# Optimization experiments

Measured on AMD Instinct MI355X. Metric: run time of the kernel, lower is better.

## Reference

```python
import jax, jax.numpy as jnp
import numpy as np

N = 8192
E = 131072
IN = 512
H = 8
C = 128
HC = H * C
EPS = 1e-5
NEG_SLOPE = 0.2


def _gatv2(x, src, dst, Wl, bl, Wr, br, att, bias):
    """GATv2Conv (PyG semantics, concat=True, self-loops already in src/dst)."""
    n = x.shape[0]
    xl = (x @ Wl + bl).reshape(n, H, C)  # source transform (lin_l)
    xr = (x @ Wr + br).reshape(n, H, C)  # dest transform (lin_r)
    m = xl[src] + xr[dst]                # [E,H,C] per-edge message
    e = jnp.einsum('ehc,hc->eh', jax.nn.leaky_relu(m, NEG_SLOPE), att)  # [E,H]
    # segment softmax over destination nodes
    emax = jax.ops.segment_max(e, dst, num_segments=n)
    w = jnp.exp(e - emax[dst])
    denom = jax.ops.segment_sum(w, dst, num_segments=n)
    alpha = w / denom[dst]               # [E,H]
    out = jax.ops.segment_sum(alpha[:, :, None] * xl[src], dst, num_segments=n)
    return out.reshape(n, HC) + bias


def _bn(x, gamma, beta):
    mu = jnp.mean(x, axis=0)
    var = jnp.mean((x - mu) ** 2, axis=0)
    return (x - mu) * jax.lax.rsqrt(var + EPS) * gamma + beta


def setup_inputs() -> dict:
    key = jax.random.key(0)
    ks = jax.random.split(key, 16)
    s = 0.05
    return {
        'x': jax.random.normal(ks[0], (N, IN), jnp.float32),
        'edge_index': jax.random.randint(ks[1], (2, E), 0, N, jnp.int32),
        'W1l': jax.random.normal(ks[2], (IN, HC), jnp.float32) * s,
        'b1l': jnp.zeros((HC,), jnp.float32),
        'W1r': jax.random.normal(ks[3], (IN, HC), jnp.float32) * s,
        'b1r': jnp.zeros((HC,), jnp.float32),
        'att1': jax.random.normal(ks[4], (H, C), jnp.float32) * s,
        'bias1': jnp.zeros((HC,), jnp.float32),
        'g1': jnp.ones((HC,), jnp.float32),
        'beta1': jnp.zeros((HC,), jnp.float32),
        'W2l': jax.random.normal(ks[5], (HC, HC), jnp.float32) * s,
        'b2l': jnp.zeros((HC,), jnp.float32),
        'W2r': jax.random.normal(ks[6], (HC, HC), jnp.float32) * s,
        'b2r': jnp.zeros((HC,), jnp.float32),
        'att2': jax.random.normal(ks[7], (H, C), jnp.float32) * s,
        'bias2': jnp.zeros((HC,), jnp.float32),
        'g2': jnp.ones((HC,), jnp.float32),
        'beta2': jnp.zeros((HC,), jnp.float32),
    }


def reference(x, edge_index, W1l, b1l, W1r, b1r, att1, bias1, g1, beta1,
              W2l, b2l, W2r, b2r, att2, bias2, g2, beta2):
    n = x.shape[0]
    loops = jnp.arange(n, dtype=edge_index.dtype)
    src = jnp.concatenate([edge_index[0], loops])
    dst = jnp.concatenate([edge_index[1], loops])
    h = _gatv2(x, src, dst, W1l, b1l, W1r, b1r, att1, bias1)
    h = jax.nn.elu(_bn(h, g1, beta1))
    h = _gatv2(h, src, dst, W2l, b2l, W2r, b2r, att2, bias2)
    h = jax.nn.elu(_bn(h, g2, beta2))
    return h
```

## Files before the change

kernel.cpp:

```cpp
#include <hip/hip_runtime.h>
#include <stdint.h>

#define NN     8192
#define NEDGE  131072
#define NETOT  (NEDGE + NN)
#define K_IN   512
#define HC_    1024
#define NOUT   2048
#define BNEPS  1e-5f
#define SLOPE  0.2f

typedef __bf16 bf16x8 __attribute__((ext_vector_type(8)));
typedef float  f32x4  __attribute__((ext_vector_type(4)));

__device__ __forceinline__ float bf2f(unsigned short u) {
  union { uint32_t u; float f; } c; c.u = ((uint32_t)u) << 16; return c.f;
}
__device__ __forceinline__ unsigned short f2bf(float f) {
  union { float f; uint32_t u; } c; c.f = f;
  uint32_t r = c.u + 0x7fffu + ((c.u >> 16) & 1u);
  return (unsigned short)(r >> 16);
}
__device__ __forceinline__ void unpack2(uint32_t u, float& lo, float& hi) {
  union { uint32_t u; float f; } a, b;
  a.u = u << 16; b.u = u & 0xffff0000u;
  lo = a.f; hi = b.f;
}

__device__ __forceinline__ void gload16(const void* g, void* l) {
  __builtin_amdgcn_global_load_lds(
      (const __attribute__((address_space(1))) uint32_t*)g,
      (__attribute__((address_space(3))) uint32_t*)l, 16, 0, 0);
}

#define SBAR() do { asm volatile("" ::: "memory"); __builtin_amdgcn_s_barrier(); asm volatile("" ::: "memory"); } while (0)

__global__ __launch_bounds__(256) void k_cvt_bf16(const float* __restrict__ in,
                                                  unsigned short* __restrict__ out, int n4) {
  int i = blockIdx.x * 256 + threadIdx.x;
  if (i >= n4) return;
  float4 v = *(const float4*)&in[(size_t)i * 4];
  ushort4 o;
  o.x = f2bf(v.x); o.y = f2bf(v.y); o.z = f2bf(v.z); o.w = f2bf(v.w);
  *(ushort4*)&out[(size_t)i * 4] = o;
}

__global__ __launch_bounds__(256) void k_transpose2_bf16(const float* __restrict__ Wa,
                                                         const float* __restrict__ Wb,
                                                         unsigned short* __restrict__ Wt,
                                                         int K, int N) {
  __shared__ float tile[32][33];
  const float* W = blockIdx.z ? Wb : Wa;
  unsigned short* dst = Wt + (size_t)blockIdx.z * N * K;
  int n0 = blockIdx.x * 32, k0 = blockIdx.y * 32;
  int tx = threadIdx.x & 31, ty = threadIdx.x >> 5;
  for (int i = ty; i < 32; i += 8)
    tile[i][tx] = W[(size_t)(k0 + i) * N + n0 + tx];
  __syncthreads();
  for (int i = ty; i < 32; i += 8)
    dst[(size_t)(n0 + i) * K + k0 + tx] = f2bf(tile[tx][i]);
}

__global__ __launch_bounds__(256) void k_hist(const int* __restrict__ ei, int* __restrict__ cnt) {
  int i = blockIdx.x * 256 + threadIdx.x;
  if (i >= NETOT) return;
  int d = (i < NEDGE) ? ei[NEDGE + i] : (i - NEDGE);
  atomicAdd(&cnt[d], 1);
}

__global__ __launch_bounds__(256) void k_scan(const int* __restrict__ cnt,
                                              int* __restrict__ rowptr,
                                              int* __restrict__ cursor) {
  __shared__ int part[256];
  int t = threadIdx.x;
  int base = t * 32;
  int s = 0;
  for (int i = 0; i < 32; ++i) s += cnt[base + i];
  part[t] = s;
  __syncthreads();
  for (int off = 1; off < 256; off <<= 1) {
    int u = (t >= off) ? part[t - off] : 0;
    __syncthreads();
    part[t] += u;
    __syncthreads();
  }
  int run = part[t] - s;
  for (int i = 0; i < 32; ++i) {
    rowptr[base + i] = run;
    cursor[base + i] = run;
    run += cnt[base + i];
  }
  if (t == 255) rowptr[NN] = run;
}

__global__ __launch_bounds__(256) void k_scatter(const int* __restrict__ ei,
                                                 int* __restrict__ cursor,
                                                 int* __restrict__ srcs) {
  int i = blockIdx.x * 256 + threadIdx.x;
  if (i >= NETOT) return;
  int s, d;
  if (i < NEDGE) { s = ei[i]; d = ei[NEDGE + i]; }
  else           { s = d = i - NEDGE; }
  int pos = atomicAdd(&cursor[d], 1);
  srcs[pos] = s;
}

__global__ __launch_bounds__(512, 2) void k_gemm256(const unsigned short* __restrict__ A,
                                                    const unsigned short* __restrict__ Bt,
                                                    const float* __restrict__ biasL,
                                                    const float* __restrict__ biasR,
                                                    unsigned short* __restrict__ C,
                                                    int K) {
  __shared__ unsigned short lA[2][256 * 64];
  __shared__ unsigned short lB[2][256 * 64];

  const int bid = blockIdx.x;
  const int xcd = bid & 7, idx = bid >> 3;
  const int m0 = (xcd * 4 + (idx & 3)) * 256;
  const int n0 = (idx >> 2) * 256;

  const int tid = threadIdx.x;
  const int l   = tid & 63;
  const int wv  = tid >> 6;
  const int wm  = wv >> 2, wn = wv & 3;
  const int l15 = l & 15, l4 = l >> 4;

  const int srow = tid >> 3;
  const int ssgk = (tid & 7) ^ (srow & 7);

  const f32x4 vzero = {0.f, 0.f, 0.f, 0.f};
  f32x4 acc[8][4];
#pragma unroll
  for (int i = 0; i < 8; ++i)
#pragma unroll
    for (int j = 0; j < 4; ++j) acc[i][j] = vzero;

  bf16x8 a2[8];
  bf16x8 bb[2][4];

  auto stageA = [&](int kt, int h) {
    const int buf = kt & 1;
    const size_t go = (size_t)(m0 + h * 128 + srow) * K + (size_t)kt * 64 + ssgk * 8;
    unsigned short* lp = &lA[buf][h * 8192 + tid * 8];
    gload16(&A[go], lp);
    gload16(&A[go + (size_t)64 * K], lp + 4096);
  };
  auto stageB = [&](int kt, int h) {
    const int buf = kt & 1;
    const size_t go = (size_t)(n0 + h * 128 + srow) * K + (size_t)kt * 64 + ssgk * 8;
    unsigned short* lp = &lB[buf][h * 8192 + tid * 8];
    gload16(&Bt[go], lp);
    gload16(&Bt[go + (size_t)64 * K], lp + 4096);
  };
  auto readA = [&](int buf, int qm) {
#pragma unroll
    for (int fm = 0; fm < 4; ++fm)
#pragma unroll
      for (int kk = 0; kk < 2; ++kk) {
        int r = wm * 128 + (qm * 4 + fm) * 16 + l15;
        int g = (kk * 4 + l4) ^ (r & 7);
        a2[fm * 2 + kk] = *(const bf16x8*)&lA[buf][r * 64 + g * 8];
      }
  };
  auto readB = [&](int buf, int qn) {
#pragma unroll
    for (int fn = 0; fn < 2; ++fn)
#pragma unroll
      for (int kk = 0; kk < 2; ++kk) {
        int r = wn * 64 + (qn * 2 + fn) * 16 + l15;
        int g = (kk * 4 + l4) ^ (r & 7);
        bb[qn][fn * 2 + kk] = *(const bf16x8*)&lB[buf][r * 64 + g * 8];
      }
  };
  auto quad = [&](int qm, int qn) {
    __builtin_amdgcn_s_setprio(1);
#pragma unroll
    for (int fm = 0; fm < 4; ++fm)
#pragma unroll
      for (int fn = 0; fn < 2; ++fn)
#pragma unroll
        for (int kk = 0; kk < 2; ++kk)
          acc[qm * 4 + fm][qn * 2 + fn] = __builtin_amdgcn_mfma_f32_16x16x32_bf16(
              a2[fm * 2 + kk], bb[qn][fn * 2 + kk], acc[qm * 4 + fm][qn * 2 + fn], 0, 0, 0);
    __builtin_amdgcn_s_setprio(0);
  };

  const int NT = K >> 6;

  stageA(0, 0); stageA(0, 1); stageB(0, 0); stageB(0, 1);
  if (NT > 1) stageA(1, 0);
  asm volatile("s_waitcnt vmcnt(2)" ::: "memory");
  SBAR();

  for (int t = 0; t < NT; ++t) {
    const int buf = t & 1;
    readA(buf, 0); readB(buf, 0);
    if (t + 1 < NT) stageA(t + 1, 1);
    SBAR();
    quad(0, 0);
    SBAR();
    readB(buf, 1);
    if (t + 1 < NT) stageB(t + 1, 0);
    SBAR();
    quad(0, 1);
    SBAR();
    readA(buf, 1);
    if (t + 1 < NT) stageB(t + 1, 1);
    SBAR();
    quad(1, 0);
    SBAR();
    if (t + 2 < NT) stageA(t + 2, 0);
    asm volatile("s_waitcnt vmcnt(2)" ::: "memory");
    SBAR();
    quad(1, 1);
    SBAR();
  }

  const float* bias = (n0 < HC_) ? biasL : (biasR - HC_);
#pragma unroll
  for (int fm = 0; fm < 8; ++fm) {
#pragma unroll
    for (int fn = 0; fn < 4; ++fn) {
      int col = n0 + wn * 64 + fn * 16 + l15;
      float bv = bias[col];
#pragma unroll
      for (int j = 0; j < 4; ++j) {
        int row = m0 + wm * 128 + fm * 16 + l4 * 4 + j;
        C[(size_t)row * NOUT + col] = f2bf(acc[fm][fn][j] + bv);
      }
    }
  }
}

template <bool OUT_BF16>
__global__ __launch_bounds__(256) void k_edge_agg(const unsigned short* __restrict__ XLR,
                                                  const float* __restrict__ att,
                                                  const float* __restrict__ bias,
                                                  const int* __restrict__ rowptr,
                                                  const int* __restrict__ srcs,
                                                  void* __restrict__ outp) {
  const int tid = threadIdx.x;
  const int d   = blockIdx.x * 4 + (tid >> 6);
  const int l   = tid & 63;
  const int c0  = l * 16;

  float attv[16], xrv[16];
  {
    const float4* ap = (const float4*)&att[c0];
#pragma unroll
    for (int q = 0; q < 4; ++q) {
      float4 v = ap[q];
      attv[q * 4 + 0] = v.x; attv[q * 4 + 1] = v.y;
      attv[q * 4 + 2] = v.z; attv[q * 4 + 3] = v.w;
    }
    const uint4* rp = (const uint4*)&XLR[(size_t)d * NOUT + HC_ + c0];
    uint4 u0 = rp[0], u1 = rp[1];
    unpack2(u0.x, xrv[0], xrv[1]);   unpack2(u0.y, xrv[2], xrv[3]);
    unpack2(u0.z, xrv[4], xrv[5]);   unpack2(u0.w, xrv[6], xrv[7]);
    unpack2(u1.x, xrv[8], xrv[9]);   unpack2(u1.y, xrv[10], xrv[11]);
    unpack2(u1.z, xrv[12], xrv[13]); unpack2(u1.w, xrv[14], xrv[15]);
  }

  float acc[16];
#pragma unroll
  for (int j = 0; j < 16; ++j) acc[j] = 0.f;
  float den = 0.f;

  const int beg = rowptr[d], end = rowptr[d + 1];
  uint4 b0u0, b0u1, b1u0, b1u1;
  {
    const uint4* rp = (const uint4*)&XLR[(size_t)srcs[beg] * NOUT + c0];
    b0u0 = rp[0]; b0u1 = rp[1];
  }
  if (beg + 1 < end) {
    const uint4* rp = (const uint4*)&XLR[(size_t)srcs[beg + 1] * NOUT + c0];
    b1u0 = rp[0]; b1u1 = rp[1];
  }
  int s2 = (beg + 2 < end) ? srcs[beg + 2] : 0;

  for (int i = beg; i < end; ++i) {
    uint4 u0 = b0u0, u1 = b0u1;
    b0u0 = b1u0; b0u1 = b1u1;
    if (i + 2 < end) {
      const uint4* rp = (const uint4*)&XLR[(size_t)s2 * NOUT + c0];
      b1u0 = rp[0]; b1u1 = rp[1];
    }
    s2 = (i + 3 < end) ? srcs[i + 3] : 0;

    float x[16];
    unpack2(u0.x, x[0], x[1]);   unpack2(u0.y, x[2], x[3]);
    unpack2(u0.z, x[4], x[5]);   unpack2(u0.w, x[6], x[7]);
    unpack2(u1.x, x[8], x[9]);   unpack2(u1.y, x[10], x[11]);
    unpack2(u1.z, x[12], x[13]); unpack2(u1.w, x[14], x[15]);
    float p = 0.f;
#pragma unroll
    for (int j = 0; j < 16; ++j) {
      float m  = x[j] + xrv[j];
      float lr = fmaxf(m, SLOPE * m);
      p = fmaf(lr, attv[j], p);
    }
    p += __shfl_xor(p, 1);
    p += __shfl_xor(p, 2);
    p += __shfl_xor(p, 4);
    float wgt = __expf(p);
    den += wgt;
#pragma unroll
    for (int j = 0; j < 16; ++j) acc[j] = fmaf(wgt, x[j], acc[j]);
  }

  float inv = 1.0f / den;
  if (OUT_BF16) {
    unsigned short* op = (unsigned short*)outp + (size_t)d * HC_ + c0;
#pragma unroll
    for (int q = 0; q < 2; ++q) {
      ushort4 o0, o1;
      const float4 bv0 = ((const float4*)&bias[c0])[q * 2];
      const float4 bv1 = ((const float4*)&bias[c0])[q * 2 + 1];
      o0.x = f2bf(acc[q * 8 + 0] * inv + bv0.x); o0.y = f2bf(acc[q * 8 + 1] * inv + bv0.y);
      o0.z = f2bf(acc[q * 8 + 2] * inv + bv0.z); o0.w = f2bf(acc[q * 8 + 3] * inv + bv0.w);
      o1.x = f2bf(acc[q * 8 + 4] * inv + bv1.x); o1.y = f2bf(acc[q * 8 + 5] * inv + bv1.y);
      o1.z = f2bf(acc[q * 8 + 6] * inv + bv1.z); o1.w = f2bf(acc[q * 8 + 7] * inv + bv1.w);
      *(ushort4*)&op[q * 8]     = o0;
      *(ushort4*)&op[q * 8 + 4] = o1;
    }
  } else {
    float* op = (float*)outp + (size_t)d * HC_ + c0;
#pragma unroll
    for (int q = 0; q < 4; ++q) {
      float4 bv = ((const float4*)&bias[c0])[q];
      float4 o = {acc[q * 4 + 0] * inv + bv.x, acc[q * 4 + 1] * inv + bv.y,
                  acc[q * 4 + 2] * inv + bv.z, acc[q * 4 + 3] * inv + bv.w};
      *(float4*)&op[q * 4] = o;
    }
  }
}

template <bool IN_BF16>
__global__ __launch_bounds__(256) void k_colstats(const void* __restrict__ Xp,
                                                  float* __restrict__ stats) {
  int col = blockIdx.x * 256 + threadIdx.x;
  int r0 = blockIdx.y * 128;
  float s = 0.f, q = 0.f;
  for (int r = r0; r < r0 + 128; ++r) {
    float v = IN_BF16 ? bf2f(((const unsigned short*)Xp)[(size_t)r * HC_ + col])
                      : ((const float*)Xp)[(size_t)r * HC_ + col];
    s += v;
    q += v * v;
  }
  atomicAdd(&stats[col], s);
  atomicAdd(&stats[HC_ + col], q);
}

template <bool IN_BF16, bool OUT_BF16>
__global__ __launch_bounds__(256) void k_bn_elu(const void* __restrict__ Xp,
                                                const float* __restrict__ stats,
                                                const float* __restrict__ gamma,
                                                const float* __restrict__ beta,
                                                void* __restrict__ outp) {
  size_t idx = (size_t)blockIdx.x * 256 + threadIdx.x;
  size_t e0 = idx * 4;
  int col = (int)(e0 & (HC_ - 1));
  float xs[4];
  if (IN_BF16) {
    ushort4 u = *(const ushort4*)&((const unsigned short*)Xp)[e0];
    xs[0] = bf2f(u.x); xs[1] = bf2f(u.y); xs[2] = bf2f(u.z); xs[3] = bf2f(u.w);
  } else {
    float4 xv = *(const float4*)&((const float*)Xp)[e0];
    xs[0] = xv.x; xs[1] = xv.y; xs[2] = xv.z; xs[3] = xv.w;
  }
  float os[4];
  const float rn = 1.0f / (float)NN;
#pragma unroll
  for (int j = 0; j < 4; ++j) {
    int c = col + j;
    float mu = stats[c] * rn;
    float var = stats[HC_ + c] * rn - mu * mu;
    float v = (xs[j] - mu) * rsqrtf(var + BNEPS) * gamma[c] + beta[c];
    os[j] = v > 0.f ? v : (__expf(v) - 1.f);
  }
  if (OUT_BF16) {
    ushort4 o;
    o.x = f2bf(os[0]); o.y = f2bf(os[1]); o.z = f2bf(os[2]); o.w = f2bf(os[3]);
    *(ushort4*)&((unsigned short*)outp)[e0] = o;
  } else {
    float4 o = {os[0], os[1], os[2], os[3]};
    *(float4*)&((float*)outp)[e0] = o;
  }
}

extern "C" void kernel_launch(void* const* d_in, const int* in_sizes, int n_in,
                              void* d_out, int out_size, void* d_ws, size_t ws_size,
                              hipStream_t stream) {
  const float* x     = (const float*)d_in[0];
  const int*   ei    = (const int*)d_in[1];
  const float* W1l   = (const float*)d_in[2];
  const float* b1l   = (const float*)d_in[3];
  const float* W1r   = (const float*)d_in[4];
  const float* b1r   = (const float*)d_in[5];
  const float* att1  = (const float*)d_in[6];
  const float* bias1 = (const float*)d_in[7];
  const float* g1    = (const float*)d_in[8];
  const float* be1   = (const float*)d_in[9];
  const float* W2l   = (const float*)d_in[10];
  const float* b2l   = (const float*)d_in[11];
  const float* W2r   = (const float*)d_in[12];
  const float* b2r   = (const float*)d_in[13];
  const float* att2  = (const float*)d_in[14];
  const float* bias2 = (const float*)d_in[15];
  const float* g2    = (const float*)d_in[16];
  const float* be2   = (const float*)d_in[17];
  float* out = (float*)d_out;

  char* wsb = (char*)d_ws;
  size_t o = 0;
  auto alloc = [&](size_t b) {
    void* p = wsb + o;
    o = (o + b + 255) & ~(size_t)255;
    return p;
  };
  unsigned short* xbf  = (unsigned short*)alloc((size_t)NN * K_IN * 2);
  unsigned short* wT1  = (unsigned short*)alloc((size_t)NOUT * K_IN * 2);
  unsigned short* wT2  = (unsigned short*)alloc((size_t)NOUT * HC_ * 2);
  unsigned short* XLR  = (unsigned short*)alloc((size_t)NN * NOUT * 2);
  unsigned short* h0   = (unsigned short*)alloc((size_t)NN * HC_ * 2);
  int* cnt     = (int*)alloc((size_t)NN * 4);
  int* rowptr  = (int*)alloc((size_t)(NN + 1) * 4);
  int* cursor  = (int*)alloc((size_t)NN * 4);
  int* srcs    = (int*)alloc((size_t)NETOT * 4);
  float* stats = (float*)alloc((size_t)2 * HC_ * 4);

  hipMemsetAsync(cnt, 0, (size_t)NN * 4, stream);
  hipMemsetAsync(stats, 0, (size_t)2 * HC_ * 4, stream);

  k_cvt_bf16<<<(NN * K_IN / 4 + 255) / 256, 256, 0, stream>>>(x, xbf, NN * K_IN / 4);
  k_transpose2_bf16<<<dim3(HC_ / 32, K_IN / 32, 2), 256, 0, stream>>>(W1l, W1r, wT1, K_IN, HC_);
  k_transpose2_bf16<<<dim3(HC_ / 32, HC_ / 32, 2), 256, 0, stream>>>(W2l, W2r, wT2, HC_, HC_);

  k_hist<<<(NETOT + 255) / 256, 256, 0, stream>>>(ei, cnt);
  k_scan<<<1, 256, 0, stream>>>(cnt, rowptr, cursor);
  k_scatter<<<(NETOT + 255) / 256, 256, 0, stream>>>(ei, cursor, srcs);

  k_gemm256<<<256, 512, 0, stream>>>(xbf, wT1, b1l, b1r, XLR, K_IN);
  k_edge_agg<true><<<NN / 4, 256, 0, stream>>>(XLR, att1, bias1, rowptr, srcs, h0);
  k_colstats<true><<<dim3(HC_ / 256, NN / 128), 256, 0, stream>>>(h0, stats);
  k_bn_elu<true, true><<<NN * HC_ / 4 / 256, 256, 0, stream>>>(h0, stats, g1, be1, h0);

  k_gemm256<<<256, 512, 0, stream>>>(h0, wT2, b2l, b2r, XLR, HC_);
  k_edge_agg<false><<<NN / 4, 256, 0, stream>>>(XLR, att2, bias2, rowptr, srcs, out);
  hipMemsetAsync(stats, 0, (size_t)2 * HC_ * 4, stream);
  k_colstats<false><<<dim3(HC_ / 256, NN / 128), 256, 0, stream>>>(out, stats);
  k_bn_elu<false, false><<<NN * HC_ / 4 / 256, 256, 0, stream>>>(out, stats, g2, be2, out);
}
```

Before: 239.9 us.

## Deepen edge-gather prefetch, use packed float2 math, store layer-2 output as bf16

The edge aggregation loop now keeps three source rows in flight instead of two, using a three-way rotated unrolled loop. It also does the leaky-relu, attention dot product and accumulation on float2 vectors so the compiler can emit packed FP32 instructions. Separately, the layer-2 aggregation writes a bf16 intermediate that colstats and bn_elu then read, which cuts memory traffic but rounds the pre-BN values to bf16. The extra prefetch depth adds register pressure.

After: 248.6 us. 1.04x slower.

```diff
diff --git a/kernel.cpp b/kernel.cpp
--- a/kernel.cpp
+++ b/kernel.cpp
@@ -12,6 +12,7 @@
 
 typedef __bf16 bf16x8 __attribute__((ext_vector_type(8)));
 typedef float  f32x4  __attribute__((ext_vector_type(4)));
+typedef float  f32x2  __attribute__((ext_vector_type(2)));
 
 __device__ __forceinline__ float bf2f(unsigned short u) {
   union { uint32_t u; float f; } c; c.u = ((uint32_t)u) << 16; return c.f;
@@ -21,10 +22,10 @@
   uint32_t r = c.u + 0x7fffu + ((c.u >> 16) & 1u);
   return (unsigned short)(r >> 16);
 }
-__device__ __forceinline__ void unpack2(uint32_t u, float& lo, float& hi) {
+__device__ __forceinline__ f32x2 upk2(uint32_t u) {
   union { uint32_t u; float f; } a, b;
   a.u = u << 16; b.u = u & 0xffff0000u;
-  lo = a.f; hi = b.f;
+  f32x2 r; r.x = a.f; r.y = b.f; return r;
 }
 
 __device__ __forceinline__ void gload16(const void* g, void* l) {
@@ -244,93 +245,102 @@
   const int l   = tid & 63;
   const int c0  = l * 16;
 
-  float attv[16], xrv[16];
+  f32x2 attv[8], xrv[8];
   {
-    const float4* ap = (const float4*)&att[c0];
-#pragma unroll
-    for (int q = 0; q < 4; ++q) {
-      float4 v = ap[q];
-      attv[q * 4 + 0] = v.x; attv[q * 4 + 1] = v.y;
-      attv[q * 4 + 2] = v.z; attv[q * 4 + 3] = v.w;
-    }
+    const f32x2* ap = (const f32x2*)&att[c0];
+#pragma unroll
+    for (int q = 0; q < 8; ++q) attv[q] = ap[q];
     const uint4* rp = (const uint4*)&XLR[(size_t)d * NOUT + HC_ + c0];
     uint4 u0 = rp[0], u1 = rp[1];
-    unpack2(u0.x, xrv[0], xrv[1]);   unpack2(u0.y, xrv[2], xrv[3]);
-    unpack2(u0.z, xrv[4], xrv[5]);   unpack2(u0.w, xrv[6], xrv[7]);
-    unpack2(u1.x, xrv[8], xrv[9]);   unpack2(u1.y, xrv[10], xrv[11]);
-    unpack2(u1.z, xrv[12], xrv[13]); unpack2(u1.w, xrv[14], xrv[15]);
-  }
-
-  float acc[16];
-#pragma unroll
-  for (int j = 0; j < 16; ++j) acc[j] = 0.f;
+    xrv[0] = upk2(u0.x); xrv[1] = upk2(u0.y); xrv[2] = upk2(u0.z); xrv[3] = upk2(u0.w);
+    xrv[4] = upk2(u1.x); xrv[5] = upk2(u1.y); xrv[6] = upk2(u1.z); xrv[7] = upk2(u1.w);
+  }
+
+  f32x2 acc[8];
+#pragma unroll
+  for (int j = 0; j < 8; ++j) acc[j] = (f32x2){0.f, 0.f};
   float den = 0.f;
 
   const int beg = rowptr[d], end = rowptr[d + 1];
-  uint4 b0u0, b0u1, b1u0, b1u1;
+
+  uint4 A0, A1, B0, B1, C0, C1;
   {
     const uint4* rp = (const uint4*)&XLR[(size_t)srcs[beg] * NOUT + c0];
-    b0u0 = rp[0]; b0u1 = rp[1];
+    A0 = rp[0]; A1 = rp[1];
   }
   if (beg + 1 < end) {
     const uint4* rp = (const uint4*)&XLR[(size_t)srcs[beg + 1] * NOUT + c0];
-    b1u0 = rp[0]; b1u1 = rp[1];
-  }
-  int s2 = (beg + 2 < end) ? srcs[beg + 2] : 0;
-
-  for (int i = beg; i < end; ++i) {
-    uint4 u0 = b0u0, u1 = b0u1;
-    b0u0 = b1u0; b0u1 = b1u1;
-    if (i + 2 < end) {
-      const uint4* rp = (const uint4*)&XLR[(size_t)s2 * NOUT + c0];
-      b1u0 = rp[0]; b1u1 = rp[1];
-    }
-    s2 = (i + 3 < end) ? srcs[i + 3] : 0;
-
-    float x[16];
-    unpack2(u0.x, x[0], x[1]);   unpack2(u0.y, x[2], x[3]);
-    unpack2(u0.z, x[4], x[5]);   unpack2(u0.w, x[6], x[7]);
-    unpack2(u1.x, x[8], x[9]);   unpack2(u1.y, x[10], x[11]);
-    unpack2(u1.z, x[12], x[13]); unpack2(u1.w, x[14], x[15]);
-    float p = 0.f;
-#pragma unroll
-    for (int j = 0; j < 16; ++j) {
-      float m  = x[j] + xrv[j];
-      float lr = fmaxf(m, SLOPE * m);
-      p = fmaf(lr, attv[j], p);
-    }
-    p += __shfl_xor(p, 1);
-    p += __shfl_xor(p, 2);
-    p += __shfl_xor(p, 4);
-    float wgt = __expf(p);
-    den += wgt;
-#pragma unroll
-    for (int j = 0; j < 16; ++j) acc[j] = fmaf(wgt, x[j], acc[j]);
-  }
+    B0 = rp[0]; B1 = rp[1];
+  }
+  if (beg + 2 < end) {
+    const uint4* rp = (const uint4*)&XLR[(size_t)srcs[beg + 2] * NOUT + c0];
+    C0 = rp[0]; C1 = rp[1];
+  }
+  int sD = (beg + 3 < end) ? srcs[beg + 3] : 0;
+  int sE = (beg + 4 < end) ? srcs[beg + 4] : 0;
+
+  int i = beg;
+
+#define EDGE_STEP(X0, X1)                                                      \
+  {                                                                            \
+    f32x2 x[8];                                                                \
+    x[0] = upk2(X0.x); x[1] = upk2(X0.y); x[2] = upk2(X0.z); x[3] = upk2(X0.w);\
+    x[4] = upk2(X1.x); x[5] = upk2(X1.y); x[6] = upk2(X1.z); x[7] = upk2(X1.w);\
+    if (i + 3 < end) {                                                         \
+      const uint4* rp = (const uint4*)&XLR[(size_t)sD * NOUT + c0];            \
+      X0 = rp[0]; X1 = rp[1];                                                  \
+    }                                                                          \
+    sD = sE;                                                                   \
+    if (i + 5 < end) sE = srcs[i + 5];                                         \
+    f32x2 ps = (f32x2){0.f, 0.f};                                              \
+    _Pragma("unroll")                                                          \
+    for (int j = 0; j < 8; ++j) {                                              \
+      f32x2 y  = x[j] + xrv[j];                                                \
+      f32x2 lr = __builtin_elementwise_max(y, y * SLOPE);                      \
+      ps = lr * attv[j] + ps;                                                  \
+    }                                                                          \
+    float p = ps.x + ps.y;                                                     \
+    p += __shfl_xor(p, 1);                                                     \
+    p += __shfl_xor(p, 2);                                                     \
+    p += __shfl_xor(p, 4);                                                     \
+    float wgt = __expf(p);                                                     \
+    den += wgt;                                                                \
+    f32x2 w2 = (f32x2){wgt, wgt};                                              \
+    _Pragma("unroll")                                                          \
+    for (int j = 0; j < 8; ++j) acc[j] = w2 * x[j] + acc[j];                   \
+    ++i;                                                                       \
+  }
+
+  while (true) {
+    EDGE_STEP(A0, A1); if (i >= end) break;
+    EDGE_STEP(B0, B1); if (i >= end) break;
+    EDGE_STEP(C0, C1); if (i >= end) break;
+  }
+#undef EDGE_STEP
 
   float inv = 1.0f / den;
+  float o[16];
+#pragma unroll
+  for (int j = 0; j < 8; ++j) {
+    f32x2 bv = ((const f32x2*)&bias[c0])[j];
+    o[j * 2]     = acc[j].x * inv + bv.x;
+    o[j * 2 + 1] = acc[j].y * inv + bv.y;
+  }
   if (OUT_BF16) {
     unsigned short* op = (unsigned short*)outp + (size_t)d * HC_ + c0;
-#pragma unroll
-    for (int q = 0; q < 2; ++q) {
-      ushort4 o0, o1;
-      const float4 bv0 = ((const float4*)&bias[c0])[q * 2];
-      const float4 bv1 = ((const float4*)&bias[c0])[q * 2 + 1];
-      o0.x = f2bf(acc[q * 8 + 0] * inv + bv0.x); o0.y = f2bf(acc[q * 8 + 1] * inv + bv0.y);
-      o0.z = f2bf(acc[q * 8 + 2] * inv + bv0.z); o0.w = f2bf(acc[q * 8 + 3] * inv + bv0.w);
-      o1.x = f2bf(acc[q * 8 + 4] * inv + bv1.x); o1.y = f2bf(acc[q * 8 + 5] * inv + bv1.y);
-      o1.z = f2bf(acc[q * 8 + 6] * inv + bv1.z); o1.w = f2bf(acc[q * 8 + 7] * inv + bv1.w);
-      *(ushort4*)&op[q * 8]     = o0;
-      *(ushort4*)&op[q * 8 + 4] = o1;
+    ushort4 u[4];
+#pragma unroll
+    for (int q = 0; q < 4; ++q) {
+      u[q].x = f2bf(o[q * 4 + 0]); u[q].y = f2bf(o[q * 4 + 1]);
+      u[q].z = f2bf(o[q * 4 + 2]); u[q].w = f2bf(o[q * 4 + 3]);
+      *(ushort4*)&op[q * 4] = u[q];
     }
   } else {
     float* op = (float*)outp + (size_t)d * HC_ + c0;
 #pragma unroll
     for (int q = 0; q < 4; ++q) {
-      float4 bv = ((const float4*)&bias[c0])[q];
-      float4 o = {acc[q * 4 + 0] * inv + bv.x, acc[q * 4 + 1] * inv + bv.y,
-                  acc[q * 4 + 2] * inv + bv.z, acc[q * 4 + 3] * inv + bv.w};
-      *(float4*)&op[q * 4] = o;
+      float4 ov = {o[q * 4 + 0], o[q * 4 + 1], o[q * 4 + 2], o[q * 4 + 3]};
+      *(float4*)&op[q * 4] = ov;
     }
   }
 }
@@ -446,8 +456,8 @@
   k_bn_elu<true, true><<<NN * HC_ / 4 / 256, 256, 0, stream>>>(h0, stats, g1, be1, h0);
 
   k_gemm256<<<256, 512, 0, stream>>>(h0, wT2, b2l, b2r, XLR, HC_);
-  k_edge_agg<false><<<NN / 4, 256, 0, stream>>>(XLR, att2, bias2, rowptr, srcs, out);
+  k_edge_agg<true><<<NN / 4, 256, 0, stream>>>(XLR, att2, bias2, rowptr, srcs, h0);
   hipMemsetAsync(stats, 0, (size_t)2 * HC_ * 4, stream);
-  k_colstats<false><<<dim3(HC_ / 256, NN / 128), 256, 0, stream>>>(out, stats);
-  k_bn_elu<false, false><<<NN * HC_ / 4 / 256, 256, 0, stream>>>(out, stats, g2, be2, out);
-}
+  k_colstats<true><<<dim3(HC_ / 256, NN / 128), 256, 0, stream>>>(h0, stats);
+  k_bn_elu<true, false><<<NN * HC_ / 4 / 256, 256, 0, stream>>>(h0, stats, g2, be2, out);
+}
```
